# Kernel optimization log

Measured on AMD Instinct MI355X. Metric: run time of the kernel, lower is better.

Reference implementation:

```python
import jax, jax.numpy as jnp
import numpy as np

B, M, E, K = 8, 256, 128, 16
H, A, R, RMS = 1024, 256, 1024, 512
NEG = -1e25


def setup_inputs() -> dict:
    key = jax.random.key(0)
    ks = jax.random.split(key, 12)
    inp = {
        "mention_reprs": jax.random.normal(ks[0], (B, M, H), jnp.float32),
        "entities": jax.random.randint(ks[1], (B, E, K), 0, M),
        "entity_masks": jax.random.randint(ks[2], (B, E, K), 0, 2, dtype=jnp.int32),
        "relation_memory": jax.random.normal(ks[3], (R, RMS), jnp.float32),
        # GatedMILAttention params
        "Wv": jax.random.normal(ks[4], (A, H), jnp.float32) / np.sqrt(H),
        "bv": jnp.zeros((A,), jnp.float32),
        "Wu": jax.random.normal(ks[5], (A, H), jnp.float32) / np.sqrt(H),
        "bu": jnp.zeros((A,), jnp.float32),
        "Wa": jax.random.normal(ks[6], (1, A), jnp.float32) / np.sqrt(A),
        "ba": jnp.zeros((1,), jnp.float32),
        # relation memory read linear: Linear(RMS, H)
        "Wr": jax.random.normal(ks[7], (H, RMS), jnp.float32) / np.sqrt(RMS),
        "br": jnp.zeros((H,), jnp.float32),
        # output linear: Linear(H + RMS, H)
        "Wo": jax.random.normal(ks[8], (H, H + RMS), jnp.float32) / np.sqrt(H + RMS),
        "bo": jnp.zeros((H,), jnp.float32),
    }
    return inp


def reference(mention_reprs, entities, entity_masks, relation_memory,
              Wv, bv, Wu, bu, Wa, ba, Wr, br, Wo, bo):
    # gather mention clusters: [B, E, K, H]
    clusters = jax.vmap(lambda m, e: m[e])(mention_reprs, entities)
    # gated MIL attention
    aV = jnp.tanh(jnp.einsum('bekh,ah->beka', clusters, Wv) + bv)
    aU = jax.nn.sigmoid(jnp.einsum('bekh,ah->beka', clusters, Wu) + bu)
    logits = jnp.einsum('beka,oa->beko', aV * aU, Wa) + ba  # [B,E,K,1]
    mask = entity_masks[..., None].astype(bool)
    logits = jnp.where(mask, logits, NEG)
    a = jax.nn.softmax(logits, axis=2)
    # weighted pooling over mentions: [B, E, H]
    entity_reprs = jnp.sum(a * clusters, axis=2)
    # relation memory read (memory detached for the read projection)
    s_w = jax.lax.stop_gradient(relation_memory) @ Wr.T + br        # [R, H]
    s = jnp.einsum('beh,rh->ber', entity_reprs, s_w)                # [B, E, R]
    s = jnp.einsum('ber,rm->bem', s, relation_memory)               # [B, E, RMS]
    out = jnp.concatenate([entity_reprs, s], axis=-1) @ Wo.T + bo   # [B, E, H]
    return out  # dropout is identity at inference
```

## Files before the change

kernel.cpp:

```cpp
#include <hip/hip_runtime.h>
#include <cstdint>
#include <cstddef>

#define NEG_ (-1e25f)

typedef __bf16 bf16x8 __attribute__((ext_vector_type(8)));
typedef float  f32x4  __attribute__((ext_vector_type(4)));
typedef short  s16x8  __attribute__((ext_vector_type(8)));
typedef const __attribute__((address_space(1))) void* gas_t;
typedef __attribute__((address_space(3))) void* las_t;

#define MFMA16 __builtin_amdgcn_mfma_f32_16x16x32_bf16

__device__ __forceinline__ short f2bf(float f) {
  union { float f; unsigned u; } v; v.f = f;
  unsigned r = v.u + 0x7fffu + ((v.u >> 16) & 1u);
  return (short)(r >> 16);
}

__device__ __forceinline__ s16x8 cvt8(const float* s) {
  bf16x8 r;
  #pragma unroll
  for (int j = 0; j < 8; ++j) r[j] = (__bf16)s[j];
  union { bf16x8 b; s16x8 s; } u; u.b = r; return u.s;
}

template <int NT>
__device__ void fgemm_dual(const float* __restrict__ A1, long lda1,
                           const float* __restrict__ A2, long lda2,
                           const float* __restrict__ B, long ldb,
                           short* __restrict__ C1, short* __restrict__ C2,
                           int ldc, int m0, int n0, short* lds) {
  const int tid = threadIdx.x, wave = tid >> 6, lane = tid & 63;
  const int quad = lane >> 4, l16 = lane & 15;
  const int wm = (wave & 1) * 32, wn = (wave >> 1) * 32;
  const int srow = tid >> 2, scol = (tid & 3) * 8;
  const float* A1g = A1 + (long)(m0 + srow) * lda1 + scol;
  const float* A2g = A2 + (long)(m0 + srow) * lda2 + scol;
  const float* Bg  = B  + (long)(n0 + srow) * ldb + scol;
  short* As1 = lds;
  short* As2 = lds + 2048;
  short* Bs  = lds + 4096;
  float r1[8], r2[8], rb[8];
  auto gload = [&](int kt) {
    long k = (long)kt * 32;
    *(float4*)(r1)     = *(const float4*)(A1g + k);
    *(float4*)(r1 + 4) = *(const float4*)(A1g + k + 4);
    *(float4*)(r2)     = *(const float4*)(A2g + k);
    *(float4*)(r2 + 4) = *(const float4*)(A2g + k + 4);
    *(float4*)(rb)     = *(const float4*)(Bg + k);
    *(float4*)(rb + 4) = *(const float4*)(Bg + k + 4);
  };
  f32x4 acc1[2][2] = {}, acc2[2][2] = {};
  gload(0);
  for (int kt = 0; kt < NT; ++kt) {
    *(s16x8*)&As1[srow * 32 + scol] = cvt8(r1);
    *(s16x8*)&As2[srow * 32 + scol] = cvt8(r2);
    *(s16x8*)&Bs[srow * 32 + scol]  = cvt8(rb);
    __syncthreads();
    if (kt + 1 < NT) gload(kt + 1);
    bf16x8 a10 = *(const bf16x8*)&As1[(wm + l16) * 32 + quad * 8];
    bf16x8 a11 = *(const bf16x8*)&As1[(wm + 16 + l16) * 32 + quad * 8];
    bf16x8 a20 = *(const bf16x8*)&As2[(wm + l16) * 32 + quad * 8];
    bf16x8 a21 = *(const bf16x8*)&As2[(wm + 16 + l16) * 32 + quad * 8];
    bf16x8 b0  = *(const bf16x8*)&Bs[(wn + l16) * 32 + quad * 8];
    bf16x8 b1  = *(const bf16x8*)&Bs[(wn + 16 + l16) * 32 + quad * 8];
    acc1[0][0] = MFMA16(a10, b0, acc1[0][0], 0, 0, 0);
    acc1[0][1] = MFMA16(a10, b1, acc1[0][1], 0, 0, 0);
    acc1[1][0] = MFMA16(a11, b0, acc1[1][0], 0, 0, 0);
    acc1[1][1] = MFMA16(a11, b1, acc1[1][1], 0, 0, 0);
    acc2[0][0] = MFMA16(a20, b0, acc2[0][0], 0, 0, 0);
    acc2[0][1] = MFMA16(a20, b1, acc2[0][1], 0, 0, 0);
    acc2[1][0] = MFMA16(a21, b0, acc2[1][0], 0, 0, 0);
    acc2[1][1] = MFMA16(a21, b1, acc2[1][1], 0, 0, 0);
    __syncthreads();
  }
  #pragma unroll
  for (int i = 0; i < 2; ++i)
    #pragma unroll
    for (int j = 0; j < 2; ++j) {
      int col = n0 + wn + j * 16 + l16;
      #pragma unroll
      for (int r = 0; r < 4; ++r) {
        int row = m0 + wm + i * 16 + quad * 4 + r;
        C1[(long)row * ldc + col] = f2bf(acc1[i][j][r]);
        C2[(long)row * ldc + col] = f2bf(acc2[i][j][r]);
      }
    }
}

template <int EPI>
__device__ void bgemm64(const short* __restrict__ A, int lda,
                        const short* __restrict__ B, int ldb,
                        void* __restrict__ C, int ldc, int NT, int m0, int n0,
                        const float* __restrict__ e0, const float* __restrict__ e1,
                        const float* __restrict__ e2, short* lds) {
  short* As = lds;
  short* Bs = lds + 4 * 2048;
  const int tid = threadIdx.x;
  const int wave = tid >> 6, lane = tid & 63;
  const int quad = lane >> 4, l16 = lane & 15;
  const int wm = (wave & 1) * 32, wn = (wave >> 1) * 32;
  const int srow = tid >> 2, scol = (tid & 3) * 8;
  const short* Ag = A + (long)(m0 + srow) * lda + scol;
  const short* Bg = B + (long)(n0 + srow) * ldb + scol;
  const int ldsoff = wave * 512;
  auto issue = [&](int kt) {
    int buf = kt & 3; int ko = kt * 32;
    __builtin_amdgcn_global_load_lds((gas_t)(Ag + ko), (las_t)(As + buf * 2048 + ldsoff), 16, 0, 0);
    __builtin_amdgcn_global_load_lds((gas_t)(Bg + ko), (las_t)(Bs + buf * 2048 + ldsoff), 16, 0, 0);
  };
  f32x4 acc[2][2] = {};
  issue(0); issue(1); issue(2);
  for (int kt = 0; kt < NT; ++kt) {
    int rem = NT - 1 - kt;
    if (rem >= 2)      asm volatile("s_waitcnt vmcnt(4)" ::: "memory");
    else if (rem == 1) asm volatile("s_waitcnt vmcnt(2)" ::: "memory");
    else               asm volatile("s_waitcnt vmcnt(0)" ::: "memory");
    asm volatile("s_barrier" ::: "memory");
    if (kt + 3 < NT) issue(kt + 3);
    const short* as = As + (kt & 3) * 2048;
    const short* bs = Bs + (kt & 3) * 2048;
    bf16x8 a0 = *(const bf16x8*)&as[(wm + l16) * 32 + quad * 8];
    bf16x8 a1 = *(const bf16x8*)&as[(wm + 16 + l16) * 32 + quad * 8];
    bf16x8 b0 = *(const bf16x8*)&bs[(wn + l16) * 32 + quad * 8];
    bf16x8 b1 = *(const bf16x8*)&bs[(wn + 16 + l16) * 32 + quad * 8];
    acc[0][0] = MFMA16(a0, b0, acc[0][0], 0, 0, 0);
    acc[0][1] = MFMA16(a0, b1, acc[0][1], 0, 0, 0);
    acc[1][0] = MFMA16(a1, b0, acc[1][0], 0, 0, 0);
    acc[1][1] = MFMA16(a1, b1, acc[1][1], 0, 0, 0);
  }
  #pragma unroll
  for (int i = 0; i < 2; ++i)
    #pragma unroll
    for (int j = 0; j < 2; ++j) {
      int col = n0 + wn + j * 16 + l16;
      #pragma unroll
      for (int r = 0; r < 4; ++r) {
        int row = m0 + wm + i * 16 + quad * 4 + r;
        float v = acc[i][j][r];
        if constexpr (EPI == 1) {
          v += e0[(long)row * 1536 + col];
          ((short*)C)[(long)row * ldc + col] = f2bf(v);
        } else {
          v += e0[col] + e1[row] * e2[col];
          ((float*)C)[(long)row * ldc + col] = v;
        }
      }
    }
}

__device__ void vu_tile(int mi, int ni, const float* __restrict__ X,
                        const float* __restrict__ Wv, const float* __restrict__ Wu,
                        const float* __restrict__ bv, const float* __restrict__ bu,
                        const float* __restrict__ Wa, float* __restrict__ wpart,
                        short* lds, float* red) {
  const int tid = threadIdx.x, wave = tid >> 6, lane = tid & 63;
  const int quad = lane >> 4, l16 = lane & 15;
  const int wm = (wave & 1) * 16, wn = (wave >> 1) * 32;
  const int m0 = mi * 32, n0 = ni * 64;
  const int srow = tid >> 2, scol = (tid & 3) * 8;
  short* As = lds;
  short* Bvs = lds + 1024;
  short* Bus = lds + 3072;
  const float* Ag  = X  + (long)(m0 + srow) * 1024 + scol;
  const float* Bvg = Wv + (long)(n0 + srow) * 1024 + scol;
  const float* Bug = Wu + (long)(n0 + srow) * 1024 + scol;
  float ra[8], rv[8], ru[8];
  auto gload = [&](int kt) {
    long k = (long)kt * 32;
    if (tid < 128) {
      *(float4*)(ra)     = *(const float4*)(Ag + k);
      *(float4*)(ra + 4) = *(const float4*)(Ag + k + 4);
    }
    *(float4*)(rv)     = *(const float4*)(Bvg + k);
    *(float4*)(rv + 4) = *(const float4*)(Bvg + k + 4);
    *(float4*)(ru)     = *(const float4*)(Bug + k);
    *(float4*)(ru + 4) = *(const float4*)(Bug + k + 4);
  };
  f32x4 accv[2] = {}, accu[2] = {};
  gload(0);
  for (int kt = 0; kt < 32; ++kt) {
    if (tid < 128) *(s16x8*)&As[srow * 32 + scol] = cvt8(ra);
    *(s16x8*)&Bvs[srow * 32 + scol] = cvt8(rv);
    *(s16x8*)&Bus[srow * 32 + scol] = cvt8(ru);
    __syncthreads();
    if (kt + 1 < 32) gload(kt + 1);
    bf16x8 af = *(const bf16x8*)&As[(wm + l16) * 32 + quad * 8];
    bf16x8 v0 = *(const bf16x8*)&Bvs[(wn + l16) * 32 + quad * 8];
    bf16x8 v1 = *(const bf16x8*)&Bvs[(wn + 16 + l16) * 32 + quad * 8];
    bf16x8 u0 = *(const bf16x8*)&Bus[(wn + l16) * 32 + quad * 8];
    bf16x8 u1 = *(const bf16x8*)&Bus[(wn + 16 + l16) * 32 + quad * 8];
    accv[0] = MFMA16(af, v0, accv[0], 0, 0, 0);
    accv[1] = MFMA16(af, v1, accv[1], 0, 0, 0);
    accu[0] = MFMA16(af, u0, accu[0], 0, 0, 0);
    accu[1] = MFMA16(af, u1, accu[1], 0, 0, 0);
    __syncthreads();
  }
  float wsum[4] = {0.f, 0.f, 0.f, 0.f};
  #pragma unroll
  for (int j = 0; j < 2; ++j) {
    int col = n0 + wn + j * 16 + l16;
    float bvc = bv[col], buc = bu[col], wac = Wa[col];
    #pragma unroll
    for (int r = 0; r < 4; ++r) {
      float vv = tanhf(accv[j][r] + bvc);
      float uu = accu[j][r] + buc;
      wsum[r] += (vv / (1.0f + expf(-uu))) * wac;
    }
  }
  #pragma unroll
  for (int r = 0; r < 4; ++r) {
    float s = wsum[r];
    s += __shfl_down(s, 8, 16);
    s += __shfl_down(s, 4, 16);
    s += __shfl_down(s, 2, 16);
    s += __shfl_down(s, 1, 16);
    if (l16 == 0) red[(wave >> 1) * 32 + wm + quad * 4 + r] = s;
  }
  __syncthreads();
  if (tid < 32) wpart[ni * 2048 + m0 + tid] = red[tid] + red[32 + tid];
}

__device__ void softmax_entity(int be, const float* __restrict__ ment,
    const int* __restrict__ ents, const int* __restrict__ msk,
    const float* __restrict__ wpart, const float* __restrict__ br,
    short* __restrict__ erb, float* __restrict__ cf,
    float* sm_a, int* sm_idx, float* sm_red) {
  const int b = be >> 7;
  const int tid = threadIdx.x;
  __syncthreads();
  if (tid < 16) {
    int idx = ents[be * 16 + tid];
    sm_idx[tid] = idx;
    int j = (b << 8) + idx;
    float lw = wpart[j] + wpart[2048 + j] + wpart[4096 + j] + wpart[6144 + j];
    sm_a[tid] = msk[be * 16 + tid] ? lw : NEG_;
  }
  __syncthreads();
  if (tid == 0) {
    float mx = sm_a[0];
    #pragma unroll
    for (int k = 1; k < 16; ++k) mx = fmaxf(mx, sm_a[k]);
    float e[16], s = 0.f;
    #pragma unroll
    for (int k = 0; k < 16; ++k) { e[k] = expf(sm_a[k] - mx); s += e[k]; }
    float inv = 1.0f / s;
    #pragma unroll
    for (int k = 0; k < 16; ++k) sm_a[k] = e[k] * inv;
  }
  __syncthreads();
  const float* Xr = ment + ((long)b << 18);
  const int h0 = tid * 4;
  float ax = 0.f, ay = 0.f, az = 0.f, aw = 0.f;
  #pragma unroll
  for (int k = 0; k < 16; ++k) {
    float ak = sm_a[k];
    float4 xv = *(const float4*)&Xr[(long)sm_idx[k] * 1024 + h0];
    ax += ak * xv.x; ay += ak * xv.y; az += ak * xv.z; aw += ak * xv.w;
  }
  short* er = erb + (long)be * 1024 + h0;
  er[0] = f2bf(ax); er[1] = f2bf(ay); er[2] = f2bf(az); er[3] = f2bf(aw);
  float4 brv = *(const float4*)&br[h0];
  float c = ax * brv.x + ay * brv.y + az * brv.z + aw * brv.w;
  #pragma unroll
  for (int off = 32; off > 0; off >>= 1) c += __shfl_down(c, off);
  if ((tid & 63) == 0) sm_red[tid >> 6] = c;
  __syncthreads();
  if (tid == 0) cf[be] = sm_red[0] + sm_red[1] + sm_red[2] + sm_red[3];
}

__global__ __launch_bounds__(256) void k1(
    const float* __restrict__ rm, const float* __restrict__ ment,
    const float* __restrict__ Wv, const float* __restrict__ Wu,
    const float* __restrict__ bv, const float* __restrict__ bu,
    const float* __restrict__ Wa, const float* __restrict__ Wr,
    const float* __restrict__ Wo, short* __restrict__ swTb,
    short* __restrict__ Ub, float* __restrict__ wpart) {
  __shared__ short lds[6144];
  __shared__ float red[64];
  const int blk = blockIdx.x;
  if (blk < 256) {
    fgemm_dual<16>(Wr, 512, Wo + 1024, 1536, rm, 512, swTb, Ub, 1024,
                   (blk >> 4) * 64, (blk & 15) * 64, lds);
  } else {
    int q = blk - 256;
    vu_tile(q & 63, q >> 6, ment, Wv, Wu, bv, bu, Wa, wpart, lds, red);
  }
}

__global__ __launch_bounds__(256) void k2(
    const short* __restrict__ Ub, const short* __restrict__ swTb,
    const float* __restrict__ Wo, const float* __restrict__ ment,
    const int* __restrict__ ents, const int* __restrict__ msk,
    const float* __restrict__ wpart, const float* __restrict__ br,
    short* __restrict__ Weffb, float* __restrict__ gw2,
    short* __restrict__ erb, float* __restrict__ cf) {
  __shared__ short lds[16384];
  __shared__ float sm_a[16];
  __shared__ int   sm_idx[16];
  __shared__ float sm_red[4];
  const int blk = blockIdx.x, tid = threadIdx.x;
  if (blk < 256) {
    bgemm64<1>(Ub, 1024, swTb, 1024, Weffb, 1024, 32,
               (blk >> 4) * 64, (blk & 15) * 64, Wo, nullptr, nullptr, lds);
  } else if (blk < 260) {
    int row = (blk - 256) * 256 + tid;
    const short* u = Ub + (long)row * 1024;
    float s = 0.f;
    for (int k = 0; k < 1024; k += 8) {
      s16x8 v = *(const s16x8*)&u[k];
      union { s16x8 s; bf16x8 b; } w; w.s = v;
      #pragma unroll
      for (int j = 0; j < 8; ++j) s += (float)w.b[j];
    }
    gw2[row] = s;
  } else {
    int s4 = (blk - 260) * 4;
    for (int e = 0; e < 4; ++e)
      softmax_entity(s4 + e, ment, ents, msk, wpart, br, erb, cf,
                     sm_a, sm_idx, sm_red);
  }
}

__global__ __launch_bounds__(256) void k3(
    const short* __restrict__ erb, const short* __restrict__ Weffb,
    const float* __restrict__ bo, const float* __restrict__ cf,
    const float* __restrict__ gw2, float* __restrict__ out) {
  __shared__ short lds[16384];
  const int blk = blockIdx.x;
  bgemm64<2>(erb, 1024, Weffb, 1024, out, 1024, 32,
             (blk >> 4) * 64, (blk & 15) * 64, bo, cf, gw2, lds);
}

extern "C" void kernel_launch(void* const* d_in, const int* in_sizes, int n_in,
                              void* d_out, int out_size, void* d_ws, size_t ws_size,
                              hipStream_t stream) {
  const float* ment = (const float*)d_in[0];
  const int*   ents = (const int*)d_in[1];
  const int*   msk  = (const int*)d_in[2];
  const float* rm   = (const float*)d_in[3];
  const float* Wv   = (const float*)d_in[4];
  const float* bv   = (const float*)d_in[5];
  const float* Wu   = (const float*)d_in[6];
  const float* bu   = (const float*)d_in[7];
  const float* Wa   = (const float*)d_in[8];
  const float* Wr   = (const float*)d_in[10];
  const float* br   = (const float*)d_in[11];
  const float* Wo   = (const float*)d_in[12];
  const float* bo   = (const float*)d_in[13];
  float* out = (float*)d_out;

  char* p = (char*)d_ws;
  auto alloc = [&](size_t bytes) {
    void* q = (void*)p; p += (bytes + 255) & ~(size_t)255; return q;
  };
  short* swTb  = (short*)alloc((size_t)1024 * 1024 * 2);
  short* Ub    = (short*)alloc((size_t)1024 * 1024 * 2);
  short* Weffb = (short*)alloc((size_t)1024 * 1024 * 2);
  short* erb   = (short*)alloc((size_t)1024 * 1024 * 2);
  float* wpart = (float*)alloc((size_t)4 * 2048 * 4);
  float* cf    = (float*)alloc((size_t)1024 * 4);
  float* gw2   = (float*)alloc((size_t)1024 * 4);

  k1<<<512, 256, 0, stream>>>(rm, ment, Wv, Wu, bv, bu, Wa, Wr, Wo,
                              swTb, Ub, wpart);
  k2<<<516, 256, 0, stream>>>(Ub, swTb, Wo, ment, ents, msk, wpart, br,
                              Weffb, gw2, erb, cf);
  k3<<<256, 256, 0, stream>>>(erb, Weffb, bo, cf, gw2, out);
}
```

Measured before the change: 140.9 us.

## Double-buffer LDS in k1 GEMMs and enlarge vu tiles to 64 rows

Both GEMM device functions in k1 now alternate between two LDS buffers and keep two register prefetch stages, which halves the number of barriers per K step and hides global-load latency further. The vu_tile path also grows from 32 to 64 mention rows per block, so Wv/Wu tiles are reused across twice as many rows and k1 launches 384 blocks instead of 512. The cost is doubled LDS and a larger register footprint, which may lower occupancy, plus fewer blocks for the vu path.

```diff
diff --git a/kernel.cpp b/kernel.cpp
--- a/kernel.cpp
+++ b/kernel.cpp
@@ -38,27 +38,21 @@
   const float* A1g = A1 + (long)(m0 + srow) * lda1 + scol;
   const float* A2g = A2 + (long)(m0 + srow) * lda2 + scol;
   const float* Bg  = B  + (long)(n0 + srow) * ldb + scol;
-  short* As1 = lds;
-  short* As2 = lds + 2048;
-  short* Bs  = lds + 4096;
-  float r1[8], r2[8], rb[8];
-  auto gload = [&](int kt) {
+  float r1e[8], r2e[8], rbe[8], r1o[8], r2o[8], rbo[8];
+  auto gloadE = [&](int kt) {
     long k = (long)kt * 32;
-    *(float4*)(r1)     = *(const float4*)(A1g + k);
-    *(float4*)(r1 + 4) = *(const float4*)(A1g + k + 4);
-    *(float4*)(r2)     = *(const float4*)(A2g + k);
-    *(float4*)(r2 + 4) = *(const float4*)(A2g + k + 4);
-    *(float4*)(rb)     = *(const float4*)(Bg + k);
-    *(float4*)(rb + 4) = *(const float4*)(Bg + k + 4);
+    *(float4*)(r1e) = *(const float4*)(A1g + k); *(float4*)(r1e + 4) = *(const float4*)(A1g + k + 4);
+    *(float4*)(r2e) = *(const float4*)(A2g + k); *(float4*)(r2e + 4) = *(const float4*)(A2g + k + 4);
+    *(float4*)(rbe) = *(const float4*)(Bg + k);  *(float4*)(rbe + 4) = *(const float4*)(Bg + k + 4);
+  };
+  auto gloadO = [&](int kt) {
+    long k = (long)kt * 32;
+    *(float4*)(r1o) = *(const float4*)(A1g + k); *(float4*)(r1o + 4) = *(const float4*)(A1g + k + 4);
+    *(float4*)(r2o) = *(const float4*)(A2g + k); *(float4*)(r2o + 4) = *(const float4*)(A2g + k + 4);
+    *(float4*)(rbo) = *(const float4*)(Bg + k);  *(float4*)(rbo + 4) = *(const float4*)(Bg + k + 4);
   };
   f32x4 acc1[2][2] = {}, acc2[2][2] = {};
-  gload(0);
-  for (int kt = 0; kt < NT; ++kt) {
-    *(s16x8*)&As1[srow * 32 + scol] = cvt8(r1);
-    *(s16x8*)&As2[srow * 32 + scol] = cvt8(r2);
-    *(s16x8*)&Bs[srow * 32 + scol]  = cvt8(rb);
-    __syncthreads();
-    if (kt + 1 < NT) gload(kt + 1);
+  auto compute = [&](const short* As1, const short* As2, const short* Bs) {
     bf16x8 a10 = *(const bf16x8*)&As1[(wm + l16) * 32 + quad * 8];
     bf16x8 a11 = *(const bf16x8*)&As1[(wm + 16 + l16) * 32 + quad * 8];
     bf16x8 a20 = *(const bf16x8*)&As2[(wm + l16) * 32 + quad * 8];
@@ -73,7 +67,20 @@
     acc2[0][1] = MFMA16(a20, b1, acc2[0][1], 0, 0, 0);
     acc2[1][0] = MFMA16(a21, b0, acc2[1][0], 0, 0, 0);
     acc2[1][1] = MFMA16(a21, b1, acc2[1][1], 0, 0, 0);
+  };
+  short* E1 = lds;          short* E2 = lds + 2048;  short* EB = lds + 4096;
+  short* O1 = lds + 6144;   short* O2 = lds + 8192;  short* OB = lds + 10240;
+  const int so = srow * 32 + scol;
+  gloadE(0); gloadO(1);
+  for (int kt = 0; kt < NT; kt += 2) {
+    *(s16x8*)&E1[so] = cvt8(r1e); *(s16x8*)&E2[so] = cvt8(r2e); *(s16x8*)&EB[so] = cvt8(rbe);
     __syncthreads();
+    if (kt + 2 < NT) gloadE(kt + 2);
+    compute(E1, E2, EB);
+    *(s16x8*)&O1[so] = cvt8(r1o); *(s16x8*)&O2[so] = cvt8(r2o); *(s16x8*)&OB[so] = cvt8(rbo);
+    __syncthreads();
+    if (kt + 3 < NT) gloadO(kt + 3);
+    compute(O1, O2, OB);
   }
   #pragma unroll
   for (int i = 0; i < 2; ++i)
@@ -157,69 +164,83 @@
                         short* lds, float* red) {
   const int tid = threadIdx.x, wave = tid >> 6, lane = tid & 63;
   const int quad = lane >> 4, l16 = lane & 15;
-  const int wm = (wave & 1) * 16, wn = (wave >> 1) * 32;
-  const int m0 = mi * 32, n0 = ni * 64;
+  const int wm = (wave & 1) * 32, wn = (wave >> 1) * 32;
+  const int m0 = mi * 64, n0 = ni * 64;
   const int srow = tid >> 2, scol = (tid & 3) * 8;
-  short* As = lds;
-  short* Bvs = lds + 1024;
-  short* Bus = lds + 3072;
   const float* Ag  = X  + (long)(m0 + srow) * 1024 + scol;
   const float* Bvg = Wv + (long)(n0 + srow) * 1024 + scol;
   const float* Bug = Wu + (long)(n0 + srow) * 1024 + scol;
-  float ra[8], rv[8], ru[8];
-  auto gload = [&](int kt) {
+  float rae[8], rve[8], rue[8], rao[8], rvo[8], ruo[8];
+  auto gloadE = [&](int kt) {
     long k = (long)kt * 32;
-    if (tid < 128) {
-      *(float4*)(ra)     = *(const float4*)(Ag + k);
-      *(float4*)(ra + 4) = *(const float4*)(Ag + k + 4);
-    }
-    *(float4*)(rv)     = *(const float4*)(Bvg + k);
-    *(float4*)(rv + 4) = *(const float4*)(Bvg + k + 4);
-    *(float4*)(ru)     = *(const float4*)(Bug + k);
-    *(float4*)(ru + 4) = *(const float4*)(Bug + k + 4);
-  };
-  f32x4 accv[2] = {}, accu[2] = {};
-  gload(0);
-  for (int kt = 0; kt < 32; ++kt) {
-    if (tid < 128) *(s16x8*)&As[srow * 32 + scol] = cvt8(ra);
-    *(s16x8*)&Bvs[srow * 32 + scol] = cvt8(rv);
-    *(s16x8*)&Bus[srow * 32 + scol] = cvt8(ru);
-    __syncthreads();
-    if (kt + 1 < 32) gload(kt + 1);
-    bf16x8 af = *(const bf16x8*)&As[(wm + l16) * 32 + quad * 8];
+    *(float4*)(rae) = *(const float4*)(Ag + k);  *(float4*)(rae + 4) = *(const float4*)(Ag + k + 4);
+    *(float4*)(rve) = *(const float4*)(Bvg + k); *(float4*)(rve + 4) = *(const float4*)(Bvg + k + 4);
+    *(float4*)(rue) = *(const float4*)(Bug + k); *(float4*)(rue + 4) = *(const float4*)(Bug + k + 4);
+  };
+  auto gloadO = [&](int kt) {
+    long k = (long)kt * 32;
+    *(float4*)(rao) = *(const float4*)(Ag + k);  *(float4*)(rao + 4) = *(const float4*)(Ag + k + 4);
+    *(float4*)(rvo) = *(const float4*)(Bvg + k); *(float4*)(rvo + 4) = *(const float4*)(Bvg + k + 4);
+    *(float4*)(ruo) = *(const float4*)(Bug + k); *(float4*)(ruo + 4) = *(const float4*)(Bug + k + 4);
+  };
+  f32x4 accv[2][2] = {}, accu[2][2] = {};
+  auto compute = [&](const short* As, const short* Bvs, const short* Bus) {
+    bf16x8 a0 = *(const bf16x8*)&As[(wm + l16) * 32 + quad * 8];
+    bf16x8 a1 = *(const bf16x8*)&As[(wm + 16 + l16) * 32 + quad * 8];
     bf16x8 v0 = *(const bf16x8*)&Bvs[(wn + l16) * 32 + quad * 8];
     bf16x8 v1 = *(const bf16x8*)&Bvs[(wn + 16 + l16) * 32 + quad * 8];
     bf16x8 u0 = *(const bf16x8*)&Bus[(wn + l16) * 32 + quad * 8];
     bf16x8 u1 = *(const bf16x8*)&Bus[(wn + 16 + l16) * 32 + quad * 8];
-    accv[0] = MFMA16(af, v0, accv[0], 0, 0, 0);
-    accv[1] = MFMA16(af, v1, accv[1], 0, 0, 0);
-    accu[0] = MFMA16(af, u0, accu[0], 0, 0, 0);
-    accu[1] = MFMA16(af, u1, accu[1], 0, 0, 0);
+    accv[0][0] = MFMA16(a0, v0, accv[0][0], 0, 0, 0);
+    accv[0][1] = MFMA16(a0, v1, accv[0][1], 0, 0, 0);
+    accv[1][0] = MFMA16(a1, v0, accv[1][0], 0, 0, 0);
+    accv[1][1] = MFMA16(a1, v1, accv[1][1], 0, 0, 0);
+    accu[0][0] = MFMA16(a0, u0, accu[0][0], 0, 0, 0);
+    accu[0][1] = MFMA16(a0, u1, accu[0][1], 0, 0, 0);
+    accu[1][0] = MFMA16(a1, u0, accu[1][0], 0, 0, 0);
+    accu[1][1] = MFMA16(a1, u1, accu[1][1], 0, 0, 0);
+  };
+  short* EA = lds;          short* EV = lds + 2048;  short* EU = lds + 4096;
+  short* OA = lds + 6144;   short* OV = lds + 8192;  short* OU = lds + 10240;
+  const int so = srow * 32 + scol;
+  gloadE(0); gloadO(1);
+  for (int kt = 0; kt < 32; kt += 2) {
+    *(s16x8*)&EA[so] = cvt8(rae); *(s16x8*)&EV[so] = cvt8(rve); *(s16x8*)&EU[so] = cvt8(rue);
     __syncthreads();
-  }
-  float wsum[4] = {0.f, 0.f, 0.f, 0.f};
-  #pragma unroll
-  for (int j = 0; j < 2; ++j) {
-    int col = n0 + wn + j * 16 + l16;
-    float bvc = bv[col], buc = bu[col], wac = Wa[col];
+    if (kt + 2 < 32) gloadE(kt + 2);
+    compute(EA, EV, EU);
+    *(s16x8*)&OA[so] = cvt8(rao); *(s16x8*)&OV[so] = cvt8(rvo); *(s16x8*)&OU[so] = cvt8(ruo);
+    __syncthreads();
+    if (kt + 3 < 32) gloadO(kt + 3);
+    compute(OA, OV, OU);
+  }
+  float wsum[2][4] = {};
+  #pragma unroll
+  for (int i = 0; i < 2; ++i)
+    #pragma unroll
+    for (int j = 0; j < 2; ++j) {
+      int col = n0 + wn + j * 16 + l16;
+      float bvc = bv[col], buc = bu[col], wac = Wa[col];
+      #pragma unroll
+      for (int r = 0; r < 4; ++r) {
+        float vv = tanhf(accv[i][j][r] + bvc);
+        float uu = accu[i][j][r] + buc;
+        wsum[i][r] += (vv / (1.0f + expf(-uu))) * wac;
+      }
+    }
+  #pragma unroll
+  for (int i = 0; i < 2; ++i)
     #pragma unroll
     for (int r = 0; r < 4; ++r) {
-      float vv = tanhf(accv[j][r] + bvc);
-      float uu = accu[j][r] + buc;
-      wsum[r] += (vv / (1.0f + expf(-uu))) * wac;
-    }
-  }
-  #pragma unroll
-  for (int r = 0; r < 4; ++r) {
-    float s = wsum[r];
-    s += __shfl_down(s, 8, 16);
-    s += __shfl_down(s, 4, 16);
-    s += __shfl_down(s, 2, 16);
-    s += __shfl_down(s, 1, 16);
-    if (l16 == 0) red[(wave >> 1) * 32 + wm + quad * 4 + r] = s;
-  }
-  __syncthreads();
-  if (tid < 32) wpart[ni * 2048 + m0 + tid] = red[tid] + red[32 + tid];
+      float s = wsum[i][r];
+      s += __shfl_down(s, 8, 16);
+      s += __shfl_down(s, 4, 16);
+      s += __shfl_down(s, 2, 16);
+      s += __shfl_down(s, 1, 16);
+      if (l16 == 0) red[(wn >> 5) * 64 + wm + i * 16 + quad * 4 + r] = s;
+    }
+  __syncthreads();
+  if (tid < 64) wpart[ni * 2048 + m0 + tid] = red[tid] + red[64 + tid];
 }
 
 __device__ void softmax_entity(int be, const float* __restrict__ ment,
@@ -277,15 +298,15 @@
     const float* __restrict__ Wa, const float* __restrict__ Wr,
     const float* __restrict__ Wo, short* __restrict__ swTb,
     short* __restrict__ Ub, float* __restrict__ wpart) {
-  __shared__ short lds[6144];
-  __shared__ float red[64];
+  __shared__ short lds[12288];
+  __shared__ float red[128];
   const int blk = blockIdx.x;
   if (blk < 256) {
     fgemm_dual<16>(Wr, 512, Wo + 1024, 1536, rm, 512, swTb, Ub, 1024,
                    (blk >> 4) * 64, (blk & 15) * 64, lds);
   } else {
     int q = blk - 256;
-    vu_tile(q & 63, q >> 6, ment, Wv, Wu, bv, bu, Wa, wpart, lds, red);
+    vu_tile(q & 31, q >> 5, ment, Wv, Wu, bv, bu, Wa, wpart, lds, red);
   }
 }
 
@@ -363,7 +384,7 @@
   float* cf    = (float*)alloc((size_t)1024 * 4);
   float* gw2   = (float*)alloc((size_t)1024 * 4);
 
-  k1<<<512, 256, 0, stream>>>(rm, ment, Wv, Wu, bv, bu, Wa, Wr, Wo,
+  k1<<<384, 256, 0, stream>>>(rm, ment, Wv, Wu, bv, bu, Wa, Wr, Wo,
                               swTb, Ub, wpart);
   k2<<<516, 256, 0, stream>>>(Ub, swTb, Wo, ment, ents, msk, wpart, br,
                               Weffb, gw2, erb, cf);
```

After: 145.2 us. 3.0% more time.
